# Optimization experiments

Hardware: AMD Instinct MI355X
Metric: run time of the kernel (lower is better)

The kernel has to match this reference:

```python
import jax, jax.numpy as jnp
import numpy as np

# --- module hyperparameters (from init_kwargs) ---
NUM_HEADS = 16
ATTN_DIM = 1024
HEAD_DIM = ATTN_DIM // NUM_HEADS  # 64
NUM_RF = 256                      # FAVOR random features per head
CONV_CH = 1024
GROUPS = 4
M_SCALE = 256                     # num_features_per_scale
GAMMAS = (0.5, 1.0, 2.0)          # gamma_list
NY_LANDMARKS = 64                 # == HEAD_DIM so shapes compose
NY_GAMMA = 1.0
EPS = 1e-6


def setup_inputs() -> dict:
    key = jax.random.key(0)
    ks = jax.random.split(key, 12)
    B, S, C = 2, 4096, CONV_CH
    G, Ms = len(GAMMAS), M_SCALE
    x = jax.random.normal(ks[0], (B, S, C), dtype=jnp.float32)
    # grouped Conv1D kernels (WIO layout): [ksize, Cin/groups, Cout], one per q/k/v
    conv_k = jax.random.normal(ks[1], (3, 3, C // GROUPS, C), jnp.float32) / np.sqrt(3 * (C // GROUPS))
    conv_b = jnp.zeros((3, C), jnp.float32)
    # multi-scale random-Fourier-feature weights per projection and per gamma scale
    rff_w = jax.random.normal(ks[2], (3, G, C, Ms), jnp.float32)
    rff_b = jax.random.uniform(ks[3], (3, G, Ms), jnp.float32) * (2.0 * np.pi)
    proj_w = jax.random.normal(ks[4], (3, G * Ms, ATTN_DIM), jnp.float32) / np.sqrt(G * Ms)
    proj_b = jnp.zeros((3, ATTN_DIM), jnp.float32)
    # FAVOR+ projection matrix (shared across heads) and Nystrom landmarks
    omega = jax.random.normal(ks[5], (HEAD_DIM, NUM_RF), jnp.float32)
    landmarks = jax.random.normal(ks[6], (NY_LANDMARKS, HEAD_DIM), jnp.float32)
    out_w = jax.random.normal(ks[7], (ATTN_DIM, ATTN_DIM), jnp.float32) / np.sqrt(ATTN_DIM)
    out_b = jnp.zeros((ATTN_DIM,), jnp.float32)
    return {"x": x, "conv_k": conv_k, "conv_b": conv_b, "rff_w": rff_w, "rff_b": rff_b,
            "proj_w": proj_w, "proj_b": proj_b, "omega": omega, "landmarks": landmarks,
            "out_w": out_w, "out_b": out_b}


def _rotary(seq_len, dh, dtype):
    inv = 1.0 / (10000.0 ** (jnp.arange(0, dh, 2, dtype=jnp.float32) / dh))
    f = jnp.arange(seq_len, dtype=jnp.float32)[:, None] * inv[None, :]  # [S, dh/2]
    emb = jnp.concatenate([f, f], axis=-1)  # [S, dh]
    return jnp.sin(emb).astype(dtype), jnp.cos(emb).astype(dtype)


def _apply_rope(x, sin, cos):
    # x: [B,H,S,D]; rotate-half RoPE
    d = x.shape[-1] // 2
    rot = jnp.concatenate([-x[..., d:], x[..., :d]], axis=-1)
    return x * cos + rot * sin


def _projection(x, ck, cb, rw, rb, pw, pb):
    # ProjectionWithKernel: grouped conv -> multi-scale RFF kernel map -> dense
    h = jax.lax.conv_general_dilated(x, ck, (1,), 'SAME',
                                     dimension_numbers=('NWC', 'WIO', 'NWC'),
                                     feature_group_count=GROUPS) + cb
    g = jnp.sqrt(2.0 * jnp.array(GAMMAS, dtype=x.dtype))[:, None]  # [G,1]
    z = jnp.cos(jnp.einsum('bsc,gcm->bsgm', h, rw) * g + rb)       # [B,S,G,Ms]
    feats = (z * jnp.sqrt(2.0 / M_SCALE)).reshape(x.shape[0], x.shape[1], -1)
    return feats @ pw + pb  # [B,S,ATTN_DIM]


def _favor(x, omega):
    # FAVOR+ positive random features: exp(x.w - |x|^2/2) / sqrt(m)
    norm = 0.5 * jnp.sum(x * x, axis=-1, keepdims=True)
    return jnp.exp(jnp.einsum('bhsd,dm->bhsm', x, omega) - norm) / jnp.sqrt(float(omega.shape[-1]))


def _nystrom(k, landmarks):
    # RBF features against landmarks (normalized by dim to keep exp in range)
    d = k.shape[-1]
    d2 = (jnp.sum(k * k, -1, keepdims=True) + jnp.sum(landmarks * landmarks, -1)
          - 2.0 * jnp.einsum('bhsd,ld->bhsl', k, landmarks))
    return jnp.exp(-NY_GAMMA * d2 / d)  # [B,H,S,L], L == HEAD_DIM


def reference(x, conv_k, conv_b, rff_w, rff_b, proj_w, proj_b, omega, landmarks, out_w, out_b):
    B, S, _ = x.shape
    qkv = [_projection(x, conv_k[i], conv_b[i], rff_w[i], rff_b[i], proj_w[i], proj_b[i])
           for i in range(3)]
    split = lambda t: t.reshape(B, S, NUM_HEADS, HEAD_DIM).transpose(0, 2, 1, 3)
    q, k, v = map(split, qkv)  # [B,H,S,Dh]
    sin, cos = _rotary(S, HEAD_DIM, x.dtype)
    q = _apply_rope(q, sin, cos)
    k = _apply_rope(k, sin, cos)
    k = _nystrom(k, landmarks)               # [B,H,S,Dh]
    qp = _favor(q, omega)                    # [B,H,S,M]
    kp = _favor(k, omega)                    # [B,H,S,M]
    denom = jnp.einsum('bhse,bhe->bhs', qp, jnp.sum(kp, axis=2))[..., None]
    kv = jnp.einsum('bhse,bhsd->bhed', kp, v)          # [B,H,M,Dh]
    num = jnp.einsum('bhse,bhed->bhsd', qp, kv)        # [B,H,S,Dh]
    out = num / (denom + EPS)
    out = out.transpose(0, 2, 1, 3).reshape(B, S, ATTN_DIM)
    return out @ out_w + out_b  # dropout is identity at inference
```

## Files before the change

kernel.cpp:

```cpp
#include <hip/hip_runtime.h>
#include <math.h>


using f32x4 = __attribute__((ext_vector_type(4))) float;
using s16x8 = __attribute__((ext_vector_type(8))) short;

__device__ __forceinline__ unsigned short f2bf(float x) {
  unsigned u = __float_as_uint(x);
  unsigned r = u + 0x7fffu + ((u >> 16) & 1u);
  return (unsigned short)(r >> 16);
}
__device__ __forceinline__ float bf2f(unsigned short h) {
  return __uint_as_float(((unsigned)h) << 16);
}

__device__ __forceinline__ void gload16(const void* g, void* l) {
  __builtin_amdgcn_global_load_lds(
      (const __attribute__((address_space(1))) void*)g,
      (__attribute__((address_space(3))) void*)l, 16, 0, 0);
}

__global__ __launch_bounds__(256) void split_prep_kernel(
    const float* __restrict__ in, unsigned short* __restrict__ ohi,
    unsigned short* __restrict__ olo, int n8)
{
  const int i = blockIdx.x * 256 + threadIdx.x;
  if (i >= n8) return;
  const float4 f0 = ((const float4*)in)[i * 2];
  const float4 f1 = ((const float4*)in)[i * 2 + 1];
  const float v[8] = {f0.x, f0.y, f0.z, f0.w, f1.x, f1.y, f1.z, f1.w};
  s16x8 hi, lo;
  #pragma unroll
  for (int u = 0; u < 8; ++u) {
    const unsigned short hh = f2bf(v[u]);
    hi[u] = (short)hh;
    lo[u] = (short)f2bf(v[u] - bf2f(hh));
  }
  ((s16x8*)ohi)[i] = hi;
  ((s16x8*)olo)[i] = lo;
}

template<int WM>
__global__ __launch_bounds__(256) void wconv_kernel(
    const float* __restrict__ in0, unsigned short* __restrict__ ohi,
    unsigned short* __restrict__ olo)
{
  int K, N;
  const float* in;
  unsigned short *oh, *ol = nullptr;
  const int z = blockIdx.z;
  if constexpr (WM == 0) {
    K = 768; N = 1024;
    in = in0 + (size_t)z * 786432;
    oh = ohi + (size_t)z * 786432; ol = olo + (size_t)z * 786432;
  } else if constexpr (WM == 1) {
    K = 1024; N = 256;
    const int i = z / 3, g = z % 3;
    in = in0 + (size_t)i * 786432 + (size_t)g * 262144;
    oh = ohi + (size_t)i * 786432 + (size_t)g * 262144;
    ol = olo + (size_t)i * 786432 + (size_t)g * 262144;
  } else if constexpr (WM == 2) {
    K = 768; N = 1024;
    in = in0 + (size_t)z * 786432; oh = ohi + (size_t)z * 786432;
  } else {
    K = 1024; N = 1024; in = in0; oh = ohi;
  }
  const int k0 = blockIdx.x * 64, n0 = blockIdx.y * 64;
  __shared__ float t[64][65];
  const int tid = threadIdx.x, tn = tid & 63, tr = tid >> 6;
  #pragma unroll 4
  for (int p = 0; p < 16; ++p) {
    const int kk = p * 4 + tr;
    t[kk][tn] = in[(size_t)(k0 + kk) * N + n0 + tn];
  }
  __syncthreads();
  #pragma unroll 4
  for (int p = 0; p < 16; ++p) {
    const int nn = p * 4 + tr;
    const float v = t[tn][nn];
    const unsigned short hi = f2bf(v);
    oh[(size_t)(n0 + nn) * K + k0 + tn] = hi;
    if constexpr (WM <= 1)
      ol[(size_t)(n0 + nn) * K + k0 + tn] = f2bf(v - bf2f(hi));
  }
}

__global__ __launch_bounds__(256) void omega_prep_kernel(
    const float* __restrict__ omega, unsigned short* __restrict__ oThi)
{
  const int idx = blockIdx.x * 256 + threadIdx.x;
  const int m = idx >> 6, d = idx & 63;
  oThi[idx] = f2bf(omega[d * 256 + m]);
}

__global__ __launch_bounds__(256) void vt_kernel(
    const float* __restrict__ V, unsigned short* __restrict__ VT)
{
  const int bh = blockIdx.x, sb = blockIdx.y;
  const int b = bh >> 4, h = bh & 15;
  __shared__ float t[64][65];
  const int tid = threadIdx.x, tn = tid & 63, tr = tid >> 6;
  #pragma unroll 4
  for (int p = 0; p < 16; ++p)
    t[p * 4 + tr][tn] =
        V[(size_t)(b * 4096 + sb * 64 + p * 4 + tr) * 1024 + h * 64 + tn];
  __syncthreads();
  #pragma unroll 4
  for (int p = 0; p < 16; ++p)
    VT[((size_t)bh * 80 + p * 4 + tr) * 4096 + sb * 64 + tn] =
        f2bf(t[tn][p * 4 + tr]);
  #pragma unroll
  for (int p = 0; p < 4; ++p) {
    const int rr = p * 4 + tr;
    VT[((size_t)bh * 80 + 64 + rr) * 4096 + sb * 64 + tn] =
        (rr == 0) ? 0x3F80 : 0;
  }
}

template<int MODE>
__global__ __launch_bounds__(256, 4) void gemm_mfma(
    const unsigned short* __restrict__ Ahi, const unsigned short* __restrict__ Alo,
    const unsigned short* __restrict__ Bhig, const unsigned short* __restrict__ Blog,
    const float* __restrict__ bias, const float2* __restrict__ tab,
    float* __restrict__ Cf, unsigned short* __restrict__ C1,
    unsigned short* __restrict__ C2,
    int M, int N, int K)
{
  constexpr bool SPLIT = (MODE <= 1);
  __shared__ alignas(16) char smem[32768];
  char* const sAhi = smem;
  char* const sAlo = smem + 8192;
  char* const sBhi = smem + (SPLIT ? 16384 : 8192);
  char* const sBlo = smem + 24576;

  const int gx = gridDim.x, gy = gridDim.y;
  const int L = blockIdx.x + gx * (blockIdx.y + gy * blockIdx.z);
  const int nwg = gx * gy * gridDim.z;
  const int logical = (L & 7) * (nwg >> 3) + (L >> 3);
  const int bx = logical % gx;
  const int by = (logical / gx) % gy;
  const int z = logical / (gx * gy);

  if constexpr (MODE == 0) {
    Bhig += (size_t)z * 786432; Blog += (size_t)z * 786432;
    bias += z * 1024;
    C1 += (size_t)z * 8388608; C2 += (size_t)z * 8388608;
  } else if constexpr (MODE == 1) {
    Ahi += (size_t)z * 8388608; Alo += (size_t)z * 8388608;
    Bhig += (size_t)z * 786432; Blog += (size_t)z * 786432;
    bias += z * 768;
    C1 += (size_t)z * 6291456;
  } else if constexpr (MODE == 2) {
    Ahi += (size_t)z * 6291456;
    Bhig += (size_t)z * 786432;
    bias += z * 1024;
    Cf += (size_t)z * 8388608;
  }

  const int tid = threadIdx.x;
  const int n0 = bx * 128;
  const int m0 = by * 128;

  const int lane = tid & 63, wid = tid >> 6;
  const int wr = wid >> 1, wc = wid & 1;
  const int fr = lane & 15, kc = lane >> 4;
  const int fsw = ((fr >> 1) & 3) << 4;

  const int seg0 = wid * 2;
  const int r0 = seg0 * 16 + (lane >> 2);
  const int r1 = r0 + 16;
  const int cp = lane & 3;
  const int c0e = (cp ^ ((r0 >> 1) & 3)) * 8;
  const int c1e = (cp ^ ((r1 >> 1) & 3)) * 8;

  f32x4 acc[4][4];
  #pragma unroll
  for (int i = 0; i < 4; ++i)
    #pragma unroll
    for (int j = 0; j < 4; ++j) acc[i][j] = f32x4{0.f, 0.f, 0.f, 0.f};

  if constexpr (SPLIT) {
    char* const dA0 = sAhi + seg0 * 1024;  char* const dA1 = dA0 + 1024;
    char* const dL0 = sAlo + seg0 * 1024;  char* const dL1 = dL0 + 1024;
    char* const dB0 = sBhi + seg0 * 1024;  char* const dB1 = dB0 + 1024;
    char* const dBl0 = sBlo + seg0 * 1024; char* const dBl1 = dBl0 + 1024;

    for (int k0 = 0; k0 < K; k0 += 32) {
      __syncthreads();
      if constexpr (MODE == 0) {
        const int t = k0 >> 8;
        const int cb = (n0 >> 8) * 256 + (k0 & 255);
        const int g0 = m0 + r0, g1 = m0 + r1;
        int s0 = (g0 & 4095) + t - 1; s0 = s0 < 0 ? 0 : (s0 > 4095 ? 4095 : s0);
        int s1 = (g1 & 4095) + t - 1; s1 = s1 < 0 ? 0 : (s1 > 4095 ? 4095 : s1);
        const size_t o0 = ((size_t)((g0 >> 12) * 4096 + s0)) * 1024 + cb;
        const size_t o1 = ((size_t)((g1 >> 12) * 4096 + s1)) * 1024 + cb;
        gload16(Ahi + o0 + c0e, dA0);
        gload16(Ahi + o1 + c1e, dA1);
        gload16(Alo + o0 + c0e, dL0);
        gload16(Alo + o1 + c1e, dL1);
      } else {
        const size_t o0 = (size_t)(m0 + r0) * K + k0;
        const size_t o1 = (size_t)(m0 + r1) * K + k0;
        gload16(Ahi + o0 + c0e, dA0);
        gload16(Ahi + o1 + c1e, dA1);
        gload16(Alo + o0 + c0e, dL0);
        gload16(Alo + o1 + c1e, dL1);
      }
      {
        const size_t o0 = (size_t)(n0 + r0) * K + k0;
        const size_t o1 = (size_t)(n0 + r1) * K + k0;
        gload16(Bhig + o0 + c0e, dB0);
        gload16(Bhig + o1 + c1e, dB1);
        gload16(Blog + o0 + c0e, dBl0);
        gload16(Blog + o1 + c1e, dBl1);
      }
      __syncthreads();

      if constexpr (MODE == 0) {
        const int t = k0 >> 8;
        int zr = -1;
        if (t == 0 && (m0 & 4095) == 0) zr = 0;
        if (t == 2 && (m0 & 4095) == 3968) zr = 127;
        if (zr >= 0) {
          if (tid < 8) {
            char* buf = (tid < 4) ? sAhi : sAlo;
            *(s16x8*)(buf + zr * 64 + (tid & 3) * 16) = s16x8{0,0,0,0,0,0,0,0};
          }
          __syncthreads();
        }
      }

      s16x8 Af[4], Al[4], Bf[4], Bl[4];
      #pragma unroll
      for (int i = 0; i < 4; ++i) {
        const int off = (wr * 64 + i * 16 + fr) * 64 + ((kc * 16) ^ fsw);
        Af[i] = *(const s16x8*)(sAhi + off);
        Al[i] = *(const s16x8*)(sAlo + off);
      }
      #pragma unroll
      for (int j = 0; j < 4; ++j) {
        const int off = (wc * 64 + j * 16 + fr) * 64 + ((kc * 16) ^ fsw);
        Bf[j] = *(const s16x8*)(sBhi + off);
        Bl[j] = *(const s16x8*)(sBlo + off);
      }
      #pragma unroll
      for (int i = 0; i < 4; ++i)
        #pragma unroll
        for (int j = 0; j < 4; ++j) {
          acc[i][j] = __builtin_amdgcn_mfma_f32_16x16x32_bf16(Af[i], Bf[j], acc[i][j], 0, 0, 0);
          acc[i][j] = __builtin_amdgcn_mfma_f32_16x16x32_bf16(Af[i], Bl[j], acc[i][j], 0, 0, 0);
          acc[i][j] = __builtin_amdgcn_mfma_f32_16x16x32_bf16(Al[i], Bf[j], acc[i][j], 0, 0, 0);
        }
    }
  } else {
    auto stagep = [&](int k0, int par) {
      char* const bA = smem + par * 16384;
      char* const bB = bA + 8192;
      const size_t o0 = (size_t)(m0 + r0) * K + k0;
      const size_t o1 = (size_t)(m0 + r1) * K + k0;
      gload16(Ahi + o0 + c0e, bA + seg0 * 1024);
      gload16(Ahi + o1 + c1e, bA + seg0 * 1024 + 1024);
      const size_t b0 = (size_t)(n0 + r0) * K + k0;
      const size_t b1 = (size_t)(n0 + r1) * K + k0;
      gload16(Bhig + b0 + c0e, bB + seg0 * 1024);
      gload16(Bhig + b1 + c1e, bB + seg0 * 1024 + 1024);
    };
    stagep(0, 0);
    __syncthreads();
    for (int k0 = 0; k0 < K; k0 += 32) {
      const int cur = (k0 >> 5) & 1;
      if (k0 + 32 < K) stagep(k0 + 32, cur ^ 1);
      const char* bA = smem + cur * 16384;
      const char* bB = bA + 8192;
      s16x8 Af[4], Bf[4];
      #pragma unroll
      for (int i = 0; i < 4; ++i) {
        const int off = (wr * 64 + i * 16 + fr) * 64 + ((kc * 16) ^ fsw);
        Af[i] = *(const s16x8*)(bA + off);
      }
      #pragma unroll
      for (int j = 0; j < 4; ++j) {
        const int off = (wc * 64 + j * 16 + fr) * 64 + ((kc * 16) ^ fsw);
        Bf[j] = *(const s16x8*)(bB + off);
      }
      #pragma unroll
      for (int i = 0; i < 4; ++i)
        #pragma unroll
        for (int j = 0; j < 4; ++j)
          acc[i][j] = __builtin_amdgcn_mfma_f32_16x16x32_bf16(Af[i], Bf[j], acc[i][j], 0, 0, 0);
      __syncthreads();
    }
  }

  if constexpr (MODE == 2) {
    #pragma unroll
    for (int i = 0; i < 4; ++i)
      #pragma unroll
      for (int j2 = 0; j2 < 2; ++j2) {
        const int col0 = n0 + wc * 64 + j2 * 16 + fr;
        const int jr = col0 & 31;
        const float b0 = bias[col0], b1 = bias[col0 + 32];
        #pragma unroll
        for (int rr = 0; rr < 4; ++rr) {
          const int row = m0 + wr * 64 + i * 16 + kc * 4 + rr;
          float v0 = acc[i][j2][rr] + b0;
          float v1 = acc[i][j2 + 2][rr] + b1;
          if (z < 2) {
            const float2 cs = tab[((row & 4095) << 5) | jr];
            const float rr0 = v0 * cs.x - v1 * cs.y;
            const float rr1 = v1 * cs.x + v0 * cs.y;
            v0 = rr0; v1 = rr1;
          }
          Cf[(size_t)row * N + col0] = v0;
          Cf[(size_t)row * N + col0 + 32] = v1;
        }
      }
  } else {
    #pragma unroll
    for (int i = 0; i < 4; ++i)
      #pragma unroll
      for (int j = 0; j < 4; ++j) {
        const int col = n0 + wc * 64 + j * 16 + fr;
        #pragma unroll
        for (int rr = 0; rr < 4; ++rr) {
          const int row = m0 + wr * 64 + i * 16 + kc * 4 + rr;
          const float v = acc[i][j][rr];
          if constexpr (MODE == 0) {
            const float hv = v + bias[col];
            const unsigned short hh = f2bf(hv);
            C1[(size_t)row * N + col] = hh;
            C2[(size_t)row * N + col] = f2bf(hv - bf2f(hh));
          } else if constexpr (MODE == 1) {
            const int g = col >> 8;
            const float sg = (g == 0) ? 1.0f : ((g == 1) ? 1.41421356237309515f : 2.0f);
            const float zc = cosf(v * sg + bias[col]) * 0.08838834764831845f;
            C1[(size_t)row * N + col] = f2bf(zc);
          } else {
            Cf[(size_t)row * N + col] = v + bias[col];
          }
        }
      }
  }
}

__global__ __launch_bounds__(256) void rope_table_kernel(float2* __restrict__ tab)
{
  const int idx = blockIdx.x * 256 + threadIdx.x;
  const int j = idx & 31, s = idx >> 5;
  const double inv = pow(10000.0, -(double)j * (1.0 / 32.0));
  double sd, cd;
  sincos((double)s * inv, &sd, &cd);
  tab[idx] = make_float2((float)cd, (float)sd);
}

__global__ __launch_bounds__(256) void nystrom_mfma(
    const float* __restrict__ Kb, const float* __restrict__ lm,
    unsigned short* __restrict__ kny, float* __restrict__ knorm)
{
  const int bid = blockIdx.x;
  const int bh = bid >> 4, chunk = bid & 15;
  const int b = bh >> 4, h = bh & 15;
  const int tid = threadIdx.x, lane = tid & 63, wid = tid >> 6;
  const int fr = lane & 15, kc = lane >> 4;
  const int ws0 = chunk * 256 + wid * 64;

  __shared__ float lnorm[64];
  if (tid < 64) {
    float s = 0.f;
    #pragma unroll
    for (int d = 0; d < 64; ++d) { const float v = lm[tid * 64 + d]; s = fmaf(v, v, s); }
    lnorm[tid] = s;
  }
  __syncthreads();

  s16x8 bfr[4][2];
  #pragma unroll
  for (int c = 0; c < 4; ++c)
    #pragma unroll
    for (int ks = 0; ks < 2; ++ks) {
      const float* lp = lm + (c * 16 + fr) * 64 + ks * 32 + kc * 8;
      #pragma unroll
      for (int u = 0; u < 8; ++u) bfr[c][ks][u] = (short)f2bf(lp[u]);
    }

  #pragma unroll
  for (int r = 0; r < 4; ++r) {
    const int s_r = ws0 + r * 16 + fr;
    const float* ap = Kb + ((size_t)(b * 4096 + s_r)) * 1024 + h * 64;
    s16x8 afr[2];
    float part = 0.f;
    #pragma unroll
    for (int ks = 0; ks < 2; ++ks) {
      const float4 f0 = *(const float4*)(ap + ks * 32 + kc * 8);
      const float4 f1 = *(const float4*)(ap + ks * 32 + kc * 8 + 4);
      const float v[8] = {f0.x, f0.y, f0.z, f0.w, f1.x, f1.y, f1.z, f1.w};
      #pragma unroll
      for (int u = 0; u < 8; ++u) {
        part = fmaf(v[u], v[u], part);
        afr[ks][u] = (short)f2bf(v[u]);
      }
    }
    part += __shfl_xor(part, 16);
    part += __shfl_xor(part, 32);

    float sq[4] = {0.f, 0.f, 0.f, 0.f};
    #pragma unroll
    for (int c = 0; c < 4; ++c) {
      f32x4 acc = f32x4{0.f, 0.f, 0.f, 0.f};
      acc = __builtin_amdgcn_mfma_f32_16x16x32_bf16(afr[0], bfr[c][0], acc, 0, 0, 0);
      acc = __builtin_amdgcn_mfma_f32_16x16x32_bf16(afr[1], bfr[c][1], acc, 0, 0, 0);
      const float ln = lnorm[c * 16 + fr];
      #pragma unroll
      for (int reg = 0; reg < 4; ++reg) {
        const float nk = __shfl(part, kc * 4 + reg);
        const float val = __expf((2.f * acc[reg] - nk - ln) * 0.015625f);
        sq[reg] = fmaf(val, val, sq[reg]);
        const int srow = ws0 + r * 16 + kc * 4 + reg;
        kny[((size_t)(b * 4096 + srow) * 16 + h) * 64 + c * 16 + fr] = f2bf(val);
      }
    }
    #pragma unroll
    for (int reg = 0; reg < 4; ++reg) {
      float s2 = sq[reg];
      s2 += __shfl_xor(s2, 1); s2 += __shfl_xor(s2, 2);
      s2 += __shfl_xor(s2, 4); s2 += __shfl_xor(s2, 8);
      if (fr == 0) {
        const int srow = ws0 + r * 16 + kc * 4 + reg;
        knorm[(size_t)(b * 4096 + srow) * 16 + h] = 0.5f * s2;
      }
    }
  }
}

__global__ __launch_bounds__(512) void favor_k_mfma(
    const unsigned short* __restrict__ kny, const float* __restrict__ knorm,
    const unsigned short* __restrict__ oThi,
    const unsigned short* __restrict__ VT, float* __restrict__ KVp)
{
  const int bid = blockIdx.x;
  const int bh = bid >> 3, chunk = bid & 7;
  const int b = bh >> 4, h = bh & 15;
  const int s0 = chunk * 512;
  const int tid = threadIdx.x, lane = tid & 63, wid = tid >> 6;
  const int fr = lane & 15, kc = lane >> 4;
  const int m0w = wid * 32;

  __shared__ unsigned short P[256][40];
  __shared__ float T[8][32][84];

  s16x8 whi[2][2];
  #pragma unroll
  for (int c = 0; c < 2; ++c)
    #pragma unroll
    for (int ks = 0; ks < 2; ++ks)
      whi[c][ks] = *(const s16x8*)(oThi + (size_t)(m0w + c * 16 + fr) * 64 + ks * 32 + kc * 8);

  f32x4 acc2[2][5];
  #pragma unroll
  for (int i = 0; i < 2; ++i)
    #pragma unroll
    for (int j = 0; j < 5; ++j) acc2[i][j] = f32x4{0.f, 0.f, 0.f, 0.f};

  for (int st = 0; st < 512; st += 32) {
    s16x8 a1[2][2];
    float nrm[2];
    #pragma unroll
    for (int r = 0; r < 2; ++r) {
      const size_t kidx = (size_t)(b * 4096 + s0 + st + r * 16 + fr) * 16 + h;
      a1[r][0] = *(const s16x8*)(kny + kidx * 64 + kc * 8);
      a1[r][1] = *(const s16x8*)(kny + kidx * 64 + 32 + kc * 8);
      nrm[r] = knorm[kidx];
    }
    __syncthreads();
    #pragma unroll
    for (int r = 0; r < 2; ++r)
      #pragma unroll
      for (int c = 0; c < 2; ++c) {
        f32x4 s1 = f32x4{0.f, 0.f, 0.f, 0.f};
        s1 = __builtin_amdgcn_mfma_f32_16x16x32_bf16(a1[r][0], whi[c][0], s1, 0, 0, 0);
        s1 = __builtin_amdgcn_mfma_f32_16x16x32_bf16(a1[r][1], whi[c][1], s1, 0, 0, 0);
        #pragma unroll
        for (int reg = 0; reg < 4; ++reg) {
          const int sl = kc * 4 + reg;
          const float nn = __shfl(nrm[r], sl);
          const float p = __expf(s1[reg] - nn - 2.772588722239781f);
          P[m0w + c * 16 + fr][r * 16 + sl] = f2bf(p);
        }
      }
    __syncthreads();
    s16x8 b2[5];
    #pragma unroll
    for (int nf = 0; nf < 5; ++nf)
      b2[nf] = *(const s16x8*)(VT + ((size_t)bh * 80 + nf * 16 + fr) * 4096 +
                               s0 + st + kc * 8);
    #pragma unroll
    for (int mf = 0; mf < 2; ++mf) {
      const s16x8 a2 = *(const s16x8*)&P[m0w + mf * 16 + fr][kc * 8];
      #pragma unroll
      for (int nf = 0; nf < 5; ++nf)
        acc2[mf][nf] = __builtin_amdgcn_mfma_f32_16x16x32_bf16(a2, b2[nf], acc2[mf][nf], 0, 0, 0);
    }
  }
  #pragma unroll
  for (int mf = 0; mf < 2; ++mf)
    #pragma unroll
    for (int nf = 0; nf < 5; ++nf)
      #pragma unroll
      for (int reg = 0; reg < 4; ++reg)
        T[wid][mf * 16 + kc * 4 + reg][nf * 16 + fr] = acc2[mf][nf][reg];
  __syncthreads();
  #pragma unroll
  for (int i = 0; i < 40; ++i) {
    const int flat = i * 64 + lane;
    const int n = flat >> 5, ml = flat & 31;
    KVp[((size_t)bid * 80 + n) * 256 + m0w + ml] = T[wid][ml][n];
  }
}

__global__ __launch_bounds__(256) void reduce_kvxt_kernel(
    const float* __restrict__ KVp, unsigned short* __restrict__ KVXT)
{
  const int bh = blockIdx.x;
  const int m = threadIdx.x;
  for (int n = 0; n < 80; ++n) {
    float s = 0.f;
    #pragma unroll
    for (int c = 0; c < 8; ++c)
      s += KVp[((size_t)(bh * 8 + c) * 80 + n) * 256 + m];
    KVXT[((size_t)bh * 80 + n) * 256 + m] = f2bf(s);
  }
}

__global__ __launch_bounds__(512) void favor_q_mfma(
    const float* __restrict__ Q, const unsigned short* __restrict__ oThi,
    const unsigned short* __restrict__ KVXT, unsigned short* __restrict__ O)
{
  const int bid = blockIdx.x;
  const int bh = bid >> 4, chunk = bid & 15;
  const int b = bh >> 4, h = bh & 15;
  const int s0 = chunk * 256;
  const int tid = threadIdx.x, lane = tid & 63, wid = tid >> 6;
  const int fr = lane & 15, kc = lane >> 4;
  const int ws0 = s0 + wid * 32;

  __shared__ unsigned short KX[80][264];
  __shared__ unsigned short P[8][32][66];

  for (int i = tid; i < 80 * 256; i += 512)
    KX[i >> 8][i & 255] = KVXT[(size_t)bh * 80 * 256 + i];
  __syncthreads();

  s16x8 ahi[2][2];
  float nrm[2];
  #pragma unroll
  for (int r = 0; r < 2; ++r) {
    float part = 0.f;
    #pragma unroll
    for (int ks = 0; ks < 2; ++ks) {
      const float* ap = Q + ((size_t)(b * 4096 + ws0 + r * 16 + fr)) * 1024 +
                        h * 64 + ks * 32 + kc * 8;
      const float4 f0 = ((const float4*)ap)[0];
      const float4 f1 = ((const float4*)ap)[1];
      const float v[8] = {f0.x, f0.y, f0.z, f0.w, f1.x, f1.y, f1.z, f1.w};
      #pragma unroll
      for (int u = 0; u < 8; ++u) {
        part = fmaf(v[u], v[u], part);
        ahi[r][ks][u] = (short)f2bf(v[u]);
      }
    }
    part += __shfl_xor(part, 16);
    part += __shfl_xor(part, 32);
    nrm[r] = 0.5f * part;
  }

  f32x4 acc2[2][5];
  #pragma unroll
  for (int i = 0; i < 2; ++i)
    #pragma unroll
    for (int j = 0; j < 5; ++j) acc2[i][j] = f32x4{0.f, 0.f, 0.f, 0.f};

  for (int mc = 0; mc < 4; ++mc) {
    __syncthreads();
    #pragma unroll
    for (int r = 0; r < 2; ++r)
      #pragma unroll
      for (int c = 0; c < 4; ++c) {
        f32x4 s1 = f32x4{0.f, 0.f, 0.f, 0.f};
        #pragma unroll
        for (int ks = 0; ks < 2; ++ks) {
          const size_t off = (size_t)(mc * 64 + c * 16 + fr) * 64 + ks * 32 + kc * 8;
          const s16x8 bh1 = *(const s16x8*)(oThi + off);
          s1 = __builtin_amdgcn_mfma_f32_16x16x32_bf16(ahi[r][ks], bh1, s1, 0, 0, 0);
        }
        #pragma unroll
        for (int reg = 0; reg < 4; ++reg) {
          const int sl = kc * 4 + reg;
          const float nn = __shfl(nrm[r], sl);
          const float p = __expf(s1[reg] - nn - 2.772588722239781f);
          P[wid][r * 16 + sl][c * 16 + fr] = f2bf(p);
        }
      }
    __syncthreads();
    #pragma unroll
    for (int ks2 = 0; ks2 < 2; ++ks2) {
      s16x8 b2[5];
      #pragma unroll
      for (int nf = 0; nf < 5; ++nf)
        b2[nf] = *(const s16x8*)&KX[nf * 16 + fr][mc * 64 + ks2 * 32 + kc * 8];
      #pragma unroll
      for (int r = 0; r < 2; ++r) {
        const s16x8 a2 = *(const s16x8*)&P[wid][r * 16 + fr][ks2 * 32 + kc * 8];
        #pragma unroll
        for (int nf = 0; nf < 5; ++nf)
          acc2[r][nf] = __builtin_amdgcn_mfma_f32_16x16x32_bf16(a2, b2[nf], acc2[r][nf], 0, 0, 0);
      }
    }
  }
  #pragma unroll
  for (int r = 0; r < 2; ++r)
    #pragma unroll
    for (int reg = 0; reg < 4; ++reg) {
      const int s = ws0 + r * 16 + kc * 4 + reg;
      const float dv = __shfl(acc2[r][4][reg], lane & 48) + 1e-6f;
      #pragma unroll
      for (int nf = 0; nf < 4; ++nf)
        O[(size_t)(b * 4096 + s) * 1024 + h * 64 + nf * 16 + fr] =
            f2bf(acc2[r][nf][reg] / dv);
    }
}

extern "C" void kernel_launch(void* const* d_in, const int* in_sizes, int n_in,
                              void* d_out, int out_size, void* d_ws, size_t ws_size,
                              hipStream_t stream)
{
  const float* x      = (const float*)d_in[0];
  const float* conv_k = (const float*)d_in[1];
  const float* conv_b = (const float*)d_in[2];
  const float* rff_w  = (const float*)d_in[3];
  const float* rff_b  = (const float*)d_in[4];
  const float* proj_w = (const float*)d_in[5];
  const float* proj_b = (const float*)d_in[6];
  const float* omega  = (const float*)d_in[7];
  const float* lm     = (const float*)d_in[8];
  const float* out_w  = (const float*)d_in[9];
  const float* out_b  = (const float*)d_in[10];

  char* wsb = (char*)d_ws;
  size_t o = 0;
  auto alloc = [&](size_t bytes) {
    char* p = wsb + o;
    o = (o + bytes + 255) & ~(size_t)255;
    return p;
  };
  unsigned short* Wc_hi = (unsigned short*)alloc(4718592);
  unsigned short* Wc_lo = (unsigned short*)alloc(4718592);
  unsigned short* Wr_hi = (unsigned short*)alloc(4718592);
  unsigned short* Wr_lo = (unsigned short*)alloc(4718592);
  unsigned short* Wp    = (unsigned short*)alloc(4718592);
  unsigned short* Wo    = (unsigned short*)alloc(2097152);
  unsigned short* oThi  = (unsigned short*)alloc(32768);
  float2* tab           = (float2*)alloc(1048576);
  char* RB = alloc(41943040);
  unsigned short* xhi   = (unsigned short*)RB;
  unsigned short* xlo   = (unsigned short*)(RB + 16777216);
  unsigned short* feats = (unsigned short*)RB;
  unsigned short* VT    = (unsigned short*)RB;
  unsigned short* Obf   = (unsigned short*)(RB + 20971520);
  unsigned short* KVXT  = (unsigned short*)(RB + 37748736);
  char* RC = alloc(100663296);
  unsigned short* hhi   = (unsigned short*)RC;
  unsigned short* hlo   = (unsigned short*)(RC + 50331648);
  float* QKV            = (float*)RC;
  char* RE = alloc(33554432);
  unsigned short* knyb  = (unsigned short*)RE;
  float* knorm          = (float*)(RE + 16777216);
  float* KVp = (float*)alloc(20971520);
  (void)ws_size;

  dim3 blk(256);
  split_prep_kernel<<<4096, blk, 0, stream>>>(x, xhi, xlo, 1048576);
  wconv_kernel<0><<<dim3(12, 16, 3), blk, 0, stream>>>(conv_k, Wc_hi, Wc_lo);
  wconv_kernel<1><<<dim3(16, 4, 9),  blk, 0, stream>>>(rff_w, Wr_hi, Wr_lo);
  wconv_kernel<2><<<dim3(12, 16, 3), blk, 0, stream>>>(proj_w, Wp, nullptr);
  wconv_kernel<3><<<dim3(16, 16, 1), blk, 0, stream>>>(out_w, Wo, nullptr);
  omega_prep_kernel<<<64, blk, 0, stream>>>(omega, oThi);
  rope_table_kernel<<<512, blk, 0, stream>>>(tab);

  gemm_mfma<0><<<dim3(8, 64, 3), blk, 0, stream>>>(
      xhi, xlo, Wc_hi, Wc_lo, conv_b, nullptr,
      nullptr, hhi, hlo, 8192, 1024, 768);
  gemm_mfma<1><<<dim3(6, 64, 3), blk, 0, stream>>>(
      hhi, hlo, Wr_hi, Wr_lo, rff_b, nullptr,
      nullptr, feats, nullptr, 8192, 768, 1024);
  gemm_mfma<2><<<dim3(8, 64, 3), blk, 0, stream>>>(
      feats, nullptr, Wp, nullptr, proj_b, tab,
      QKV, nullptr, nullptr, 8192, 1024, 768);

  float* Qb = QKV;
  float* Kb = QKV + 8388608;
  float* Vb = QKV + 16777216;
  vt_kernel<<<dim3(32, 64), blk, 0, stream>>>(Vb, VT);
  nystrom_mfma<<<512, blk, 0, stream>>>(Kb, lm, knyb, knorm);
  favor_k_mfma<<<256, dim3(512), 0, stream>>>(knyb, knorm, oThi, VT, KVp);
  reduce_kvxt_kernel<<<32, blk, 0, stream>>>(KVp, KVXT);
  favor_q_mfma<<<512, dim3(512), 0, stream>>>(Qb, oThi, KVXT, Obf);
  gemm_mfma<3><<<dim3(8, 64, 1), blk, 0, stream>>>(
      Obf, nullptr, Wo, nullptr, out_b, nullptr,
      (float*)d_out, nullptr, nullptr, 8192, 1024, 1024);
}
```

Measured before the change: 908.4 us.

## Store QKV as bf16, merge prep kernels, parallelize KV reduction

The QKV projection epilogue now writes bf16 instead of fp32, and the downstream V-transpose, Nystrom and FAVOR-Q kernels read bf16 directly. This halves that intermediate's write and read traffic and removes repeated conversions. Norms are now computed from the rounded bf16 values, which changes numerics slightly. The seven small prep launches are folded into two kernels, and the KV reduction gets a second grid dimension so more blocks share the work.

```diff
diff --git a/kernel.cpp b/kernel.cpp
--- a/kernel.cpp
+++ b/kernel.cpp
@@ -20,53 +20,75 @@
       (__attribute__((address_space(3))) void*)l, 16, 0, 0);
 }
 
-__global__ __launch_bounds__(256) void split_prep_kernel(
-    const float* __restrict__ in, unsigned short* __restrict__ ohi,
-    unsigned short* __restrict__ olo, int n8)
-{
-  const int i = blockIdx.x * 256 + threadIdx.x;
-  if (i >= n8) return;
-  const float4 f0 = ((const float4*)in)[i * 2];
-  const float4 f1 = ((const float4*)in)[i * 2 + 1];
-  const float v[8] = {f0.x, f0.y, f0.z, f0.w, f1.x, f1.y, f1.z, f1.w};
-  s16x8 hi, lo;
-  #pragma unroll
-  for (int u = 0; u < 8; ++u) {
-    const unsigned short hh = f2bf(v[u]);
-    hi[u] = (short)hh;
-    lo[u] = (short)f2bf(v[u] - bf2f(hh));
-  }
-  ((s16x8*)ohi)[i] = hi;
-  ((s16x8*)olo)[i] = lo;
-}
-
-template<int WM>
-__global__ __launch_bounds__(256) void wconv_kernel(
-    const float* __restrict__ in0, unsigned short* __restrict__ ohi,
-    unsigned short* __restrict__ olo)
-{
-  int K, N;
+__global__ __launch_bounds__(256) void misc_prep_kernel(
+    const float* __restrict__ x, unsigned short* __restrict__ xhi,
+    unsigned short* __restrict__ xlo,
+    const float* __restrict__ omega, unsigned short* __restrict__ oThi,
+    float2* __restrict__ tab)
+{
+  const int fid = blockIdx.x, tid = threadIdx.x;
+  if (fid < 4096) {
+    const int i = fid * 256 + tid;
+    const float4 f0 = ((const float4*)x)[i * 2];
+    const float4 f1 = ((const float4*)x)[i * 2 + 1];
+    const float v[8] = {f0.x, f0.y, f0.z, f0.w, f1.x, f1.y, f1.z, f1.w};
+    s16x8 hi, lo;
+    #pragma unroll
+    for (int u = 0; u < 8; ++u) {
+      const unsigned short hh = f2bf(v[u]);
+      hi[u] = (short)hh;
+      lo[u] = (short)f2bf(v[u] - bf2f(hh));
+    }
+    ((s16x8*)xhi)[i] = hi;
+    ((s16x8*)xlo)[i] = lo;
+  } else if (fid < 4160) {
+    const int idx = (fid - 4096) * 256 + tid;
+    const int m = idx >> 6, d = idx & 63;
+    oThi[idx] = f2bf(omega[d * 256 + m]);
+  } else {
+    const int idx = (fid - 4160) * 256 + tid;
+    const int j = idx & 31, s = idx >> 5;
+    const double inv = pow(10000.0, -(double)j * (1.0 / 32.0));
+    double sd, cd;
+    sincos((double)s * inv, &sd, &cd);
+    tab[idx] = make_float2((float)cd, (float)sd);
+  }
+}
+
+__global__ __launch_bounds__(256) void wprep_kernel(
+    const float* __restrict__ conv_k, const float* __restrict__ rff_w,
+    const float* __restrict__ proj_w, const float* __restrict__ out_w,
+    unsigned short* __restrict__ Wc_hi, unsigned short* __restrict__ Wc_lo,
+    unsigned short* __restrict__ Wr_hi, unsigned short* __restrict__ Wr_lo,
+    unsigned short* __restrict__ Wp, unsigned short* __restrict__ Wo)
+{
+  __shared__ float t[64][65];
+  const int fid = blockIdx.x;
   const float* in;
   unsigned short *oh, *ol = nullptr;
-  const int z = blockIdx.z;
-  if constexpr (WM == 0) {
-    K = 768; N = 1024;
-    in = in0 + (size_t)z * 786432;
-    oh = ohi + (size_t)z * 786432; ol = olo + (size_t)z * 786432;
-  } else if constexpr (WM == 1) {
-    K = 1024; N = 256;
-    const int i = z / 3, g = z % 3;
-    in = in0 + (size_t)i * 786432 + (size_t)g * 262144;
-    oh = ohi + (size_t)i * 786432 + (size_t)g * 262144;
-    ol = olo + (size_t)i * 786432 + (size_t)g * 262144;
-  } else if constexpr (WM == 2) {
-    K = 768; N = 1024;
-    in = in0 + (size_t)z * 786432; oh = ohi + (size_t)z * 786432;
+  int K, N, k0, n0;
+  if (fid < 576) {
+    const int z = fid / 192, r = fid % 192;
+    K = 768; N = 1024; k0 = (r % 12) * 64; n0 = (r / 12) * 64;
+    in = conv_k + (size_t)z * 786432;
+    oh = Wc_hi + (size_t)z * 786432; ol = Wc_lo + (size_t)z * 786432;
+  } else if (fid < 1152) {
+    const int q = fid - 576;
+    const int zz = q / 64, r = q % 64;
+    K = 1024; N = 256; k0 = (r % 16) * 64; n0 = (r / 16) * 64;
+    const int i = zz / 3, g = zz % 3;
+    const size_t off = (size_t)i * 786432 + (size_t)g * 262144;
+    in = rff_w + off; oh = Wr_hi + off; ol = Wr_lo + off;
+  } else if (fid < 1728) {
+    const int q = fid - 1152;
+    const int z = q / 192, r = q % 192;
+    K = 768; N = 1024; k0 = (r % 12) * 64; n0 = (r / 12) * 64;
+    in = proj_w + (size_t)z * 786432; oh = Wp + (size_t)z * 786432;
   } else {
-    K = 1024; N = 1024; in = in0; oh = ohi;
-  }
-  const int k0 = blockIdx.x * 64, n0 = blockIdx.y * 64;
-  __shared__ float t[64][65];
+    const int q = fid - 1728;
+    K = 1024; N = 1024; k0 = (q % 16) * 64; n0 = (q / 16) * 64;
+    in = out_w; oh = Wo;
+  }
   const int tid = threadIdx.x, tn = tid & 63, tr = tid >> 6;
   #pragma unroll 4
   for (int p = 0; p < 16; ++p) {
@@ -80,25 +102,16 @@
     const float v = t[tn][nn];
     const unsigned short hi = f2bf(v);
     oh[(size_t)(n0 + nn) * K + k0 + tn] = hi;
-    if constexpr (WM <= 1)
-      ol[(size_t)(n0 + nn) * K + k0 + tn] = f2bf(v - bf2f(hi));
-  }
-}
-
-__global__ __launch_bounds__(256) void omega_prep_kernel(
-    const float* __restrict__ omega, unsigned short* __restrict__ oThi)
-{
-  const int idx = blockIdx.x * 256 + threadIdx.x;
-  const int m = idx >> 6, d = idx & 63;
-  oThi[idx] = f2bf(omega[d * 256 + m]);
+    if (ol) ol[(size_t)(n0 + nn) * K + k0 + tn] = f2bf(v - bf2f(hi));
+  }
 }
 
 __global__ __launch_bounds__(256) void vt_kernel(
-    const float* __restrict__ V, unsigned short* __restrict__ VT)
+    const unsigned short* __restrict__ V, unsigned short* __restrict__ VT)
 {
   const int bh = blockIdx.x, sb = blockIdx.y;
   const int b = bh >> 4, h = bh & 15;
-  __shared__ float t[64][65];
+  __shared__ unsigned t[64][65];
   const int tid = threadIdx.x, tn = tid & 63, tr = tid >> 6;
   #pragma unroll 4
   for (int p = 0; p < 16; ++p)
@@ -108,7 +121,7 @@
   #pragma unroll 4
   for (int p = 0; p < 16; ++p)
     VT[((size_t)bh * 80 + p * 4 + tr) * 4096 + sb * 64 + tn] =
-        f2bf(t[tn][p * 4 + tr]);
+        (unsigned short)t[tn][p * 4 + tr];
   #pragma unroll
   for (int p = 0; p < 4; ++p) {
     const int rr = p * 4 + tr;
@@ -154,7 +167,7 @@
     Ahi += (size_t)z * 6291456;
     Bhig += (size_t)z * 786432;
     bias += z * 1024;
-    Cf += (size_t)z * 8388608;
+    C1 += (size_t)z * 8388608;
   }
 
   const int tid = threadIdx.x;
@@ -312,8 +325,8 @@
             const float rr1 = v1 * cs.x + v0 * cs.y;
             v0 = rr0; v1 = rr1;
           }
-          Cf[(size_t)row * N + col0] = v0;
-          Cf[(size_t)row * N + col0 + 32] = v1;
+          C1[(size_t)row * N + col0] = f2bf(v0);
+          C1[(size_t)row * N + col0 + 32] = f2bf(v1);
         }
       }
   } else {
@@ -344,18 +357,8 @@
   }
 }
 
-__global__ __launch_bounds__(256) void rope_table_kernel(float2* __restrict__ tab)
-{
-  const int idx = blockIdx.x * 256 + threadIdx.x;
-  const int j = idx & 31, s = idx >> 5;
-  const double inv = pow(10000.0, -(double)j * (1.0 / 32.0));
-  double sd, cd;
-  sincos((double)s * inv, &sd, &cd);
-  tab[idx] = make_float2((float)cd, (float)sd);
-}
-
 __global__ __launch_bounds__(256) void nystrom_mfma(
-    const float* __restrict__ Kb, const float* __restrict__ lm,
+    const unsigned short* __restrict__ Kb, const float* __restrict__ lm,
     unsigned short* __restrict__ kny, float* __restrict__ knorm)
 {
   const int bid = blockIdx.x;
@@ -387,18 +390,16 @@
   #pragma unroll
   for (int r = 0; r < 4; ++r) {
     const int s_r = ws0 + r * 16 + fr;
-    const float* ap = Kb + ((size_t)(b * 4096 + s_r)) * 1024 + h * 64;
+    const unsigned short* ap = Kb + ((size_t)(b * 4096 + s_r)) * 1024 + h * 64;
     s16x8 afr[2];
     float part = 0.f;
     #pragma unroll
     for (int ks = 0; ks < 2; ++ks) {
-      const float4 f0 = *(const float4*)(ap + ks * 32 + kc * 8);
-      const float4 f1 = *(const float4*)(ap + ks * 32 + kc * 8 + 4);
-      const float v[8] = {f0.x, f0.y, f0.z, f0.w, f1.x, f1.y, f1.z, f1.w};
+      afr[ks] = *(const s16x8*)(ap + ks * 32 + kc * 8);
       #pragma unroll
       for (int u = 0; u < 8; ++u) {
-        part = fmaf(v[u], v[u], part);
-        afr[ks][u] = (short)f2bf(v[u]);
+        const float v = bf2f((unsigned short)afr[ks][u]);
+        part = fmaf(v, v, part);
       }
     }
     part += __shfl_xor(part, 16);
@@ -522,8 +523,10 @@
     const float* __restrict__ KVp, unsigned short* __restrict__ KVXT)
 {
   const int bh = blockIdx.x;
+  const int n0 = blockIdx.y * 8;
   const int m = threadIdx.x;
-  for (int n = 0; n < 80; ++n) {
+  #pragma unroll
+  for (int n = n0; n < n0 + 8; ++n) {
     float s = 0.f;
     #pragma unroll
     for (int c = 0; c < 8; ++c)
@@ -533,7 +536,7 @@
 }
 
 __global__ __launch_bounds__(512) void favor_q_mfma(
-    const float* __restrict__ Q, const unsigned short* __restrict__ oThi,
+    const unsigned short* __restrict__ Q, const unsigned short* __restrict__ oThi,
     const unsigned short* __restrict__ KVXT, unsigned short* __restrict__ O)
 {
   const int bid = blockIdx.x;
@@ -556,17 +559,14 @@
   #pragma unroll
   for (int r = 0; r < 2; ++r) {
     float part = 0.f;
+    const unsigned short* ap = Q + ((size_t)(b * 4096 + ws0 + r * 16 + fr)) * 1024 + h * 64;
     #pragma unroll
     for (int ks = 0; ks < 2; ++ks) {
-      const float* ap = Q + ((size_t)(b * 4096 + ws0 + r * 16 + fr)) * 1024 +
-                        h * 64 + ks * 32 + kc * 8;
-      const float4 f0 = ((const float4*)ap)[0];
-      const float4 f1 = ((const float4*)ap)[1];
-      const float v[8] = {f0.x, f0.y, f0.z, f0.w, f1.x, f1.y, f1.z, f1.w};
+      ahi[r][ks] = *(const s16x8*)(ap + ks * 32 + kc * 8);
       #pragma unroll
       for (int u = 0; u < 8; ++u) {
-        part = fmaf(v[u], v[u], part);
-        ahi[r][ks][u] = (short)f2bf(v[u]);
+        const float v = bf2f((unsigned short)ahi[r][ks][u]);
+        part = fmaf(v, v, part);
       }
     }
     part += __shfl_xor(part, 16);
@@ -671,7 +671,7 @@
   char* RC = alloc(100663296);
   unsigned short* hhi   = (unsigned short*)RC;
   unsigned short* hlo   = (unsigned short*)(RC + 50331648);
-  float* QKV            = (float*)RC;
+  unsigned short* QKV   = (unsigned short*)RC;
   char* RE = alloc(33554432);
   unsigned short* knyb  = (unsigned short*)RE;
   float* knorm          = (float*)(RE + 16777216);
@@ -679,13 +679,9 @@
   (void)ws_size;
 
   dim3 blk(256);
-  split_prep_kernel<<<4096, blk, 0, stream>>>(x, xhi, xlo, 1048576);
-  wconv_kernel<0><<<dim3(12, 16, 3), blk, 0, stream>>>(conv_k, Wc_hi, Wc_lo);
-  wconv_kernel<1><<<dim3(16, 4, 9),  blk, 0, stream>>>(rff_w, Wr_hi, Wr_lo);
-  wconv_kernel<2><<<dim3(12, 16, 3), blk, 0, stream>>>(proj_w, Wp, nullptr);
-  wconv_kernel<3><<<dim3(16, 16, 1), blk, 0, stream>>>(out_w, Wo, nullptr);
-  omega_prep_kernel<<<64, blk, 0, stream>>>(omega, oThi);
-  rope_table_kernel<<<512, blk, 0, stream>>>(tab);
+  misc_prep_kernel<<<4672, blk, 0, stream>>>(x, xhi, xlo, omega, oThi, tab);
+  wprep_kernel<<<1984, blk, 0, stream>>>(conv_k, rff_w, proj_w, out_w,
+                                         Wc_hi, Wc_lo, Wr_hi, Wr_lo, Wp, Wo);
 
   gemm_mfma<0><<<dim3(8, 64, 3), blk, 0, stream>>>(
       xhi, xlo, Wc_hi, Wc_lo, conv_b, nullptr,
@@ -695,15 +691,15 @@
       nullptr, feats, nullptr, 8192, 768, 1024);
   gemm_mfma<2><<<dim3(8, 64, 3), blk, 0, stream>>>(
       feats, nullptr, Wp, nullptr, proj_b, tab,
-      QKV, nullptr, nullptr, 8192, 1024, 768);
-
-  float* Qb = QKV;
-  float* Kb = QKV + 8388608;
-  float* Vb = QKV + 16777216;
+      nullptr, QKV, nullptr, 8192, 1024, 768);
+
+  unsigned short* Qb = QKV;
+  unsigned short* Kb = QKV + 8388608;
+  unsigned short* Vb = QKV + 16777216;
   vt_kernel<<<dim3(32, 64), blk, 0, stream>>>(Vb, VT);
   nystrom_mfma<<<512, blk, 0, stream>>>(Kb, lm, knyb, knorm);
   favor_k_mfma<<<256, dim3(512), 0, stream>>>(knyb, knorm, oThi, VT, KVp);
-  reduce_kvxt_kernel<<<32, blk, 0, stream>>>(KVp, KVXT);
+  reduce_kvxt_kernel<<<dim3(32, 10), blk, 0, stream>>>(KVp, KVXT);
   favor_q_mfma<<<512, dim3(512), 0, stream>>>(Qb, oThi, KVXT, Obf);
   gemm_mfma<3><<<dim3(8, 64, 1), blk, 0, stream>>>(
       Obf, nullptr, Wo, nullptr, out_b, nullptr,
```

Result: faster. 877.1 us (-3.4%).
